# Performance work log

Measured on AMD Instinct MI355X. Metric: run time of the kernel, lower is better.

The kernel has to match this reference:

```python
import jax, jax.numpy as jnp
import numpy as np

H, D = 8, 32  # gat_num_heads, structure_feature_dim // heads
N_CFG, E_CFG = 20000, 320000
N_DFG, E_DFG = 20000, 320000


def _gat(x, src, dst, lin, a_s, a_d, b):
    # PyG GATConv (concat=True), inference (dropout off). src/dst include self-loops.
    N = x.shape[0]
    xw = (x @ lin).reshape(N, H, D)              # [N,H,D]
    sc_s = (xw * a_s).sum(-1)                    # [N,H] att_src scores
    sc_d = (xw * a_d).sum(-1)                    # [N,H] att_dst scores
    alpha = jax.nn.leaky_relu(sc_s[src] + sc_d[dst], 0.2)   # [E,H]
    m = jax.lax.stop_gradient(jax.ops.segment_max(alpha, dst, num_segments=N))
    e = jnp.exp(alpha - m[dst])
    s = jax.ops.segment_sum(e, dst, num_segments=N)
    w = e / s[dst]                               # softmax over incoming edges per dst
    out = jax.ops.segment_sum(xw[src] * w[..., None], dst, num_segments=N)
    return out.reshape(N, H * D) + b


def _gat_stack(x, ei, params):
    N = x.shape[0]
    loops = jnp.arange(N)
    src = jnp.concatenate([ei[0], loops])        # add_self_loops=True (PyG default)
    dst = jnp.concatenate([ei[1], loops])
    for p in params:
        x = jax.nn.relu(_gat(x, src, dst, *p))
    return x.mean(0, keepdims=True)              # global_mean_pool -> [1, 256]


def _mha(x, in_w, in_b, out_w, out_b):
    # torch nn.MultiheadAttention, seq_len=1, batch=1, x:[1,256]
    qkv = x @ in_w.T + in_b                      # [1, 3*256]
    q, k, v = jnp.split(qkv, 3, axis=-1)
    q = q.reshape(1, H, D); k = k.reshape(1, H, D); v = v.reshape(1, H, D)
    scores = (q * k).sum(-1, keepdims=True) / jnp.sqrt(jnp.float32(D))
    attn = jax.nn.softmax(scores, axis=0)        # key length 1
    return (attn * v).reshape(1, H * D) @ out_w.T + out_b


def setup_inputs():
    key = jax.random.key(0)
    ks = iter(jax.random.split(key, 40))
    d = {}
    d['cfg_x'] = jax.random.normal(next(ks), (N_CFG, 64), jnp.float32)
    d['dfg_x'] = jax.random.normal(next(ks), (N_DFG, 32), jnp.float32)
    d['cfg_ei'] = jax.random.randint(next(ks), (2, E_CFG), 0, N_CFG)
    d['dfg_ei'] = jax.random.randint(next(ks), (2, E_DFG), 0, N_DFG)
    for name, in0 in (('cfg', 64), ('dfg', 32)):
        for i in range(3):
            fi = in0 if i == 0 else H * D
            s = 1.0 / np.sqrt(fi)
            d[f'{name}_lin{i}'] = jax.random.normal(next(ks), (fi, H * D), jnp.float32) * s
            d[f'{name}_as{i}'] = jax.random.normal(next(ks), (H, D), jnp.float32) * s
            d[f'{name}_ad{i}'] = jax.random.normal(next(ks), (H, D), jnp.float32) * s
            d[f'{name}_b{i}'] = jnp.zeros((H * D,), jnp.float32)
    E = H * D
    d['mha_in_w'] = jax.random.normal(next(ks), (3 * E, E), jnp.float32) / np.sqrt(E)
    d['mha_in_b'] = jnp.zeros((3 * E,), jnp.float32)
    d['mha_out_w'] = jax.random.normal(next(ks), (E, E), jnp.float32) / np.sqrt(E)
    d['mha_out_b'] = jnp.zeros((E,), jnp.float32)
    d['fus_w'] = jax.random.normal(next(ks), (E, 2 * E), jnp.float32) / np.sqrt(2 * E)
    d['fus_b'] = jnp.zeros((E,), jnp.float32)
    return d


def reference(cfg_x, dfg_x, cfg_ei, dfg_ei,
              cfg_lin0, cfg_as0, cfg_ad0, cfg_b0,
              cfg_lin1, cfg_as1, cfg_ad1, cfg_b1,
              cfg_lin2, cfg_as2, cfg_ad2, cfg_b2,
              dfg_lin0, dfg_as0, dfg_ad0, dfg_b0,
              dfg_lin1, dfg_as1, dfg_ad1, dfg_b1,
              dfg_lin2, dfg_as2, dfg_ad2, dfg_b2,
              mha_in_w, mha_in_b, mha_out_w, mha_out_b, fus_w, fus_b):
    cfg_p = [(cfg_lin0, cfg_as0, cfg_ad0, cfg_b0),
             (cfg_lin1, cfg_as1, cfg_ad1, cfg_b1),
             (cfg_lin2, cfg_as2, cfg_ad2, cfg_b2)]
    dfg_p = [(dfg_lin0, dfg_as0, dfg_ad0, dfg_b0),
             (dfg_lin1, dfg_as1, dfg_ad1, dfg_b1),
             (dfg_lin2, dfg_as2, dfg_ad2, dfg_b2)]
    cfg_f = _mha(_gat_stack(cfg_x, cfg_ei, cfg_p), mha_in_w, mha_in_b, mha_out_w, mha_out_b)
    dfg_f = _mha(_gat_stack(dfg_x, dfg_ei, dfg_p), mha_in_w, mha_in_b, mha_out_w, mha_out_b)
    return jnp.concatenate([cfg_f, dfg_f], axis=1) @ fus_w.T + fus_b
```

## Files before the change

kernel.cpp:

```cpp
#include <hip/hip_runtime.h>

#define NN 20000
#define ER 320000
#define ET 340000
#define CC 256
#define HH 8
#define DD 32


__global__ void zero_k(int* cnt, float* pooled) {
  int t = blockIdx.x * 256 + threadIdx.x;
  if (t < NN) cnt[t] = 0;
  if (pooled && t < 2 * CC) pooled[t] = 0.f;
}


__global__ void hist_k(const int* __restrict__ ei, int* __restrict__ cnt) {
  int e = blockIdx.x * 256 + threadIdx.x;
  if (e >= ET) return;
  int dst = (e < ER) ? ei[ER + e] : (e - ER);
  atomicAdd(&cnt[dst], 1);
}

__global__ __launch_bounds__(1024) void scan_k(const int* __restrict__ cnt,
                                               int* __restrict__ offs,
                                               int* __restrict__ cur) {
  __shared__ int part[1024];
  int t = threadIdx.x;
  const int CH = (NN + 1023) / 1024;
  int b = t * CH; if (b > NN) b = NN;
  int e = b + CH; if (e > NN) e = NN;
  int s = 0;
  for (int i = b; i < e; ++i) s += cnt[i];
  part[t] = s;
  __syncthreads();
  for (int off = 1; off < 1024; off <<= 1) {
    int v = (t >= off) ? part[t - off] : 0;
    __syncthreads();
    part[t] += v;
    __syncthreads();
  }
  int run = (t > 0) ? part[t - 1] : 0;
  for (int i = b; i < e; ++i) {
    int c = cnt[i];
    offs[i] = run;
    cur[i] = run;
    run += c;
  }
  if (t == 0) offs[NN] = ET;
}

__global__ void scatter_k(const int* __restrict__ ei, int* __restrict__ cur,
                          int* __restrict__ csr_src, int* __restrict__ csr_dst) {
  int e = blockIdx.x * 256 + threadIdx.x;
  if (e >= ET) return;
  int src, dst;
  if (e < ER) { src = ei[e]; dst = ei[ER + e]; }
  else        { src = dst = e - ER; }
  int pos = atomicAdd(&cur[dst], 1);
  csr_src[pos] = src;
  csr_dst[pos] = dst;
}

__global__ __launch_bounds__(256) void gemm_k(const float* __restrict__ X,
                                              const float* __restrict__ W,
                                              float* __restrict__ O, int K) {
  __shared__ float As[2][16][68];
  __shared__ float Bs[2][16][68];
  int tid = threadIdx.x;
  int tx = tid & 15;
  int ty = tid >> 4;
  int rb = blockIdx.y * 64, cb = blockIdx.x * 64;

  int arow = tid & 63;
  int akc = (tid >> 6) * 4;
  int bkk = tid >> 4;
  int bcol = (tid & 15) * 4;
  int gr = rb + arow; if (gr >= NN) gr = NN - 1;

  float acc[4][4] = {};
  float4 ar, br;
  int nk = K >> 4;

#define GLOAD(k0)                                                     \
  do {                                                                \
    ar = *(const float4*)&X[(size_t)gr * K + (k0) + akc];             \
    br = *(const float4*)&W[(size_t)((k0) + bkk) * CC + cb + bcol];   \
  } while (0)

#define LWRITE(buf)                                                   \
  do {                                                                \
    As[buf][akc][arow] = ar.x; As[buf][akc + 1][arow] = ar.y;         \
    As[buf][akc + 2][arow] = ar.z; As[buf][akc + 3][arow] = ar.w;     \
    *(float4*)&Bs[buf][bkk][bcol] = br;                               \
  } while (0)

  GLOAD(0);
  LWRITE(0);
  __syncthreads();
  int cur = 0;
  for (int t = 0; t < nk; ++t) {
    if (t + 1 < nk) GLOAD((t + 1) << 4);
#pragma unroll
    for (int kk = 0; kk < 16; ++kk) {
      float4 a = *(const float4*)&As[cur][kk][ty * 4];
      float4 b = *(const float4*)&Bs[cur][kk][tx * 4];
      acc[0][0] += a.x * b.x; acc[0][1] += a.x * b.y; acc[0][2] += a.x * b.z; acc[0][3] += a.x * b.w;
      acc[1][0] += a.y * b.x; acc[1][1] += a.y * b.y; acc[1][2] += a.y * b.z; acc[1][3] += a.y * b.w;
      acc[2][0] += a.z * b.x; acc[2][1] += a.z * b.y; acc[2][2] += a.z * b.z; acc[2][3] += a.z * b.w;
      acc[3][0] += a.w * b.x; acc[3][1] += a.w * b.y; acc[3][2] += a.w * b.z; acc[3][3] += a.w * b.w;
    }
    if (t + 1 < nk) LWRITE(cur ^ 1);
    __syncthreads();
    cur ^= 1;
  }
#undef GLOAD
#undef LWRITE

#pragma unroll
  for (int i = 0; i < 4; ++i) {
    int r = rb + ty * 4 + i;
    if (r < NN) {
      *(float4*)&O[(size_t)r * CC + cb + tx * 4] =
          make_float4(acc[i][0], acc[i][1], acc[i][2], acc[i][3]);
    }
  }
}

__global__ void scores_k(const float* __restrict__ xw, const float* __restrict__ a_s,
                         const float* __restrict__ a_d, float* __restrict__ scs,
                         float* __restrict__ scd) {
  int t = blockIdx.x * blockDim.x + threadIdx.x;
  if (t >= NN * HH) return;
  int h = t & 7, n = t >> 3;
  const float* row = xw + (size_t)n * CC + h * DD;
  const float* as = a_s + h * DD;
  const float* ad = a_d + h * DD;
  float ss = 0.f, sd = 0.f;
#pragma unroll
  for (int d = 0; d < DD; ++d) {
    float v = row[d];
    ss += v * as[d];
    sd += v * ad[d];
  }
  scs[t] = ss;
  scd[t] = sd;
}

__global__ void alpha_k(const int* __restrict__ csr_src, const int* __restrict__ csr_dst,
                        const float* __restrict__ scs, const float* __restrict__ scd,
                        float* __restrict__ alpha) {
  int p = blockIdx.x * 256 + threadIdx.x;
  if (p >= ET) return;
  int s = csr_src[p], d = csr_dst[p];
  const float4* s4 = (const float4*)(scs + (size_t)s * 8);
  const float4* d4 = (const float4*)(scd + (size_t)d * 8);
  float4 a0 = s4[0], a1 = s4[1];
  float4 b0 = d4[0], b1 = d4[1];
  float4 r0, r1;
  float v;
  v = a0.x + b0.x; r0.x = v > 0.f ? v : 0.2f * v;
  v = a0.y + b0.y; r0.y = v > 0.f ? v : 0.2f * v;
  v = a0.z + b0.z; r0.z = v > 0.f ? v : 0.2f * v;
  v = a0.w + b0.w; r0.w = v > 0.f ? v : 0.2f * v;
  v = a1.x + b1.x; r1.x = v > 0.f ? v : 0.2f * v;
  v = a1.y + b1.y; r1.y = v > 0.f ? v : 0.2f * v;
  v = a1.z + b1.z; r1.z = v > 0.f ? v : 0.2f * v;
  v = a1.w + b1.w; r1.w = v > 0.f ? v : 0.2f * v;
  float4* o4 = (float4*)(alpha + (size_t)p * 8);
  o4[0] = r0; o4[1] = r1;
}

__global__ __launch_bounds__(256) void stats_k(const float* __restrict__ alpha,
                                               const int* __restrict__ offs,
                                               float* __restrict__ ms,
                                               float* __restrict__ inv) {
  int wid = (blockIdx.x * 256 + threadIdx.x) >> 6;
  if (wid >= NN) return;
  int lane = threadIdx.x & 63;
  int j = lane >> 3, h = lane & 7;
  int beg = offs[wid], end = offs[wid + 1];
  float m = -1e30f;
  for (int p = beg + j; p < end; p += 8)
    m = fmaxf(m, alpha[(size_t)p * 8 + h]);
#pragma unroll
  for (int off = 8; off <= 32; off <<= 1)
    m = fmaxf(m, __shfl_xor(m, off, 64));
  float s = 0.f;
  for (int p = beg + j; p < end; p += 8)
    s += __expf(alpha[(size_t)p * 8 + h] - m);
#pragma unroll
  for (int off = 8; off <= 32; off <<= 1)
    s += __shfl_xor(s, off, 64);
  if (lane < 8) {
    ms[(size_t)wid * 8 + h] = m;
    inv[(size_t)wid * 8 + h] = 1.f / s;
  }
}

__global__ __launch_bounds__(256) void aggr_k(const float* __restrict__ xw,
                                              const float* __restrict__ alpha,
                                              const float* __restrict__ ms,
                                              const float* __restrict__ inv,
                                              const int* __restrict__ csr,
                                              const int* __restrict__ offs,
                                              const float* __restrict__ bias,
                                              float* __restrict__ out) {
  int n = blockIdx.x;
  int tid = threadIdx.x;
  int h = tid >> 5;
  int beg = offs[n], end = offs[n + 1];
  float m = ms[(size_t)n * 8 + h];
  float iv = inv[(size_t)n * 8 + h];
  float acc = 0.f;
  int p = beg;
  for (; p + 8 <= end; p += 8) {
    int s[8]; float wv[8]; float x[8];
#pragma unroll
    for (int i = 0; i < 8; ++i) s[i] = csr[p + i];
#pragma unroll
    for (int i = 0; i < 8; ++i) wv[i] = alpha[(size_t)(p + i) * 8 + h];
#pragma unroll
    for (int i = 0; i < 8; ++i) x[i] = xw[(size_t)s[i] * CC + tid];
#pragma unroll
    for (int i = 0; i < 8; ++i) acc += __expf(wv[i] - m) * iv * x[i];
  }
  for (; p + 4 <= end; p += 4) {
    int s[4]; float wv[4]; float x[4];
#pragma unroll
    for (int i = 0; i < 4; ++i) s[i] = csr[p + i];
#pragma unroll
    for (int i = 0; i < 4; ++i) wv[i] = alpha[(size_t)(p + i) * 8 + h];
#pragma unroll
    for (int i = 0; i < 4; ++i) x[i] = xw[(size_t)s[i] * CC + tid];
#pragma unroll
    for (int i = 0; i < 4; ++i) acc += __expf(wv[i] - m) * iv * x[i];
  }
  for (; p < end; ++p)
    acc += __expf(alpha[(size_t)p * 8 + h] - m) * iv * xw[(size_t)csr[p] * CC + tid];
  float r = acc + bias[tid];
  out[(size_t)n * CC + tid] = (r > 0.f) ? r : 0.f;
}

__global__ void pool_k(const float* __restrict__ x, float* __restrict__ pooled) {
  int tid = threadIdx.x;
  int rb = blockIdx.x * 50;
  float acc = 0.f;
  for (int r = 0; r < 50; ++r) acc += x[(size_t)(rb + r) * CC + tid];
  atomicAdd(&pooled[tid], acc * (1.f / NN));
}

__global__ __launch_bounds__(256) void head12_k(const float* __restrict__ x,
                                                const float* __restrict__ W,
                                                const float* __restrict__ b,
                                                float* __restrict__ y) {
  int o = (blockIdx.x * 256 + threadIdx.x) >> 6;
  if (o >= 512) return;
  int lane = threadIdx.x & 63;
  int g = o >> 8, t = o & 255;
  float4 wv = *(const float4*)&W[(size_t)t * 256 + lane * 4];
  float4 xv = *(const float4*)&x[g * 256 + lane * 4];
  float s = wv.x * xv.x + wv.y * xv.y + wv.z * xv.z + wv.w * xv.w;
#pragma unroll
  for (int off = 32; off >= 1; off >>= 1) s += __shfl_xor(s, off, 64);
  if (lane == 0) y[o] = s + b[t];
}

__global__ __launch_bounds__(256) void head3_k(const float* __restrict__ f,
                                               const float* __restrict__ W,
                                               const float* __restrict__ b,
                                               float* __restrict__ out) {
  int o = (blockIdx.x * 256 + threadIdx.x) >> 6;
  if (o >= 256) return;
  int lane = threadIdx.x & 63;
  const float* wr = W + (size_t)o * 512;
  float4 w0 = *(const float4*)&wr[lane * 4];
  float4 w1 = *(const float4*)&wr[lane * 4 + 256];
  float4 f0 = *(const float4*)&f[lane * 4];
  float4 f1 = *(const float4*)&f[lane * 4 + 256];
  float s = w0.x * f0.x + w0.y * f0.y + w0.z * f0.z + w0.w * f0.w +
            w1.x * f1.x + w1.y * f1.y + w1.z * f1.z + w1.w * f1.w;
#pragma unroll
  for (int off = 32; off >= 1; off >>= 1) s += __shfl_xor(s, off, 64);
  if (lane == 0) out[o] = s + b[o];
}

extern "C" void kernel_launch(void* const* d_in, const int* in_sizes, int n_in,
                              void* d_out, int out_size, void* d_ws, size_t ws_size,
                              hipStream_t stream) {
  const float* cfg_x = (const float*)d_in[0];
  const float* dfg_x = (const float*)d_in[1];
  const int* cfg_ei = (const int*)d_in[2];
  const int* dfg_ei = (const int*)d_in[3];
  const float *lin[2][3], *as_[2][3], *ad_[2][3], *bs_[2][3];
  for (int g = 0; g < 2; ++g)
    for (int i = 0; i < 3; ++i) {
      int base = 4 + g * 12 + i * 4;
      lin[g][i] = (const float*)d_in[base];
      as_[g][i] = (const float*)d_in[base + 1];
      ad_[g][i] = (const float*)d_in[base + 2];
      bs_[g][i] = (const float*)d_in[base + 3];
    }
  const float* mha_in_w = (const float*)d_in[28];
  const float* mha_in_b = (const float*)d_in[29];
  const float* mha_out_w = (const float*)d_in[30];
  const float* mha_out_b = (const float*)d_in[31];
  const float* fus_w = (const float*)d_in[32];
  const float* fus_b = (const float*)d_in[33];
  float* outp = (float*)d_out;

  char* w = (char*)d_ws;
  size_t o = 0;
  auto alloc = [&](size_t bytes) -> char* {
    char* p = w + o;
    o += (bytes + 255) & ~(size_t)255;
    return p;
  };
  float* bufA = (float*)alloc((size_t)NN * CC * 4);
  float* bufB = (float*)alloc((size_t)NN * CC * 4);
  float* scs = (float*)alloc((size_t)NN * HH * 4);
  float* scd = (float*)alloc((size_t)NN * HH * 4);
  float* ms = (float*)alloc((size_t)NN * HH * 4);
  float* inv = (float*)alloc((size_t)NN * HH * 4);
  float* alpha = (float*)alloc((size_t)ET * HH * 4);
  int* csr = (int*)alloc((size_t)ET * 4);
  int* csrd = (int*)alloc((size_t)ET * 4);
  int* offs = (int*)alloc((size_t)(NN + 1) * 4);
  int* cnt = (int*)alloc((size_t)NN * 4);
  int* cur = (int*)alloc((size_t)NN * 4);
  float* pooled = (float*)alloc(2 * CC * 4);
  float* vbuf = (float*)alloc(2 * CC * 4);
  float* fbuf = (float*)alloc(2 * CC * 4);

  const int* ei[2] = {cfg_ei, dfg_ei};
  const float* xin[2] = {cfg_x, dfg_x};
  const int K0[2] = {64, 32};

  for (int g = 0; g < 2; ++g) {
    zero_k<<<(NN + 255) / 256, 256, 0, stream>>>(cnt, g == 0 ? pooled : nullptr);
    hist_k<<<(ET + 255) / 256, 256, 0, stream>>>(ei[g], cnt);
    scan_k<<<1, 1024, 0, stream>>>(cnt, offs, cur);
    scatter_k<<<(ET + 255) / 256, 256, 0, stream>>>(ei[g], cur, csr, csrd);

    const float* x = xin[g];
    for (int l = 0; l < 3; ++l) {
      int K = (l == 0) ? K0[g] : CC;
      dim3 grid(CC / 64, (NN + 63) / 64);
      gemm_k<<<grid, 256, 0, stream>>>(x, lin[g][l], bufA, K);
      scores_k<<<(NN * HH + 255) / 256, 256, 0, stream>>>(bufA, as_[g][l], ad_[g][l],
                                                          scs, scd);
      alpha_k<<<(ET + 255) / 256, 256, 0, stream>>>(csr, csrd, scs, scd, alpha);
      stats_k<<<(NN * 64 + 255) / 256, 256, 0, stream>>>(alpha, offs, ms, inv);
      aggr_k<<<NN, 256, 0, stream>>>(bufA, alpha, ms, inv, csr, offs, bs_[g][l], bufB);
      x = bufB;
    }
    pool_k<<<(NN / 50), 256, 0, stream>>>(bufB, pooled + g * CC);
  }
  head12_k<<<128, 256, 0, stream>>>(pooled, mha_in_w + 512 * 256, mha_in_b + 512, vbuf);
  head12_k<<<128, 256, 0, stream>>>(vbuf, mha_out_w, mha_out_b, fbuf);
  head3_k<<<64, 256, 0, stream>>>(fbuf, fus_w, fus_b, outp);
}
```

Baseline: 930.9 us.

## Fuse attention scores into GEMM epilogue and alpha computation into softmax stats

Computes the per-head source and destination attention scores in the GEMM epilogue with warp shuffles, which removes the separate scores kernel and its re-read of the projected features. The leaky-relu alpha computation moves into the per-destination stats kernel, gathering source scores through the CSR, so the alpha kernel and the csr_dst array are no longer needed. This drops two launches per layer and some memory traffic. In exchange, the stats kernel now does scattered gathers, and the GEMM epilogue relies on each head's 32 columns mapping onto 8 adjacent lanes.

```diff
diff --git a/kernel.cpp b/kernel.cpp
--- a/kernel.cpp
+++ b/kernel.cpp
@@ -51,7 +51,7 @@
 }
 
 __global__ void scatter_k(const int* __restrict__ ei, int* __restrict__ cur,
-                          int* __restrict__ csr_src, int* __restrict__ csr_dst) {
+                          int* __restrict__ csr_src) {
   int e = blockIdx.x * 256 + threadIdx.x;
   if (e >= ET) return;
   int src, dst;
@@ -59,12 +59,15 @@
   else        { src = dst = e - ER; }
   int pos = atomicAdd(&cur[dst], 1);
   csr_src[pos] = src;
-  csr_dst[pos] = dst;
 }
 
 __global__ __launch_bounds__(256) void gemm_k(const float* __restrict__ X,
                                               const float* __restrict__ W,
-                                              float* __restrict__ O, int K) {
+                                              float* __restrict__ O, int K,
+                                              const float* __restrict__ a_s,
+                                              const float* __restrict__ a_d,
+                                              float* __restrict__ scs,
+                                              float* __restrict__ scd) {
   __shared__ float As[2][16][68];
   __shared__ float Bs[2][16][68];
   int tid = threadIdx.x;
@@ -125,54 +128,39 @@
           make_float4(acc[i][0], acc[i][1], acc[i][2], acc[i][3]);
     }
   }
-}
-
-__global__ void scores_k(const float* __restrict__ xw, const float* __restrict__ a_s,
-                         const float* __restrict__ a_d, float* __restrict__ scs,
-                         float* __restrict__ scd) {
-  int t = blockIdx.x * blockDim.x + threadIdx.x;
-  if (t >= NN * HH) return;
-  int h = t & 7, n = t >> 3;
-  const float* row = xw + (size_t)n * CC + h * DD;
-  const float* as = a_s + h * DD;
-  const float* ad = a_d + h * DD;
-  float ss = 0.f, sd = 0.f;
-#pragma unroll
-  for (int d = 0; d < DD; ++d) {
-    float v = row[d];
-    ss += v * as[d];
-    sd += v * ad[d];
-  }
-  scs[t] = ss;
-  scd[t] = sd;
-}
-
-__global__ void alpha_k(const int* __restrict__ csr_src, const int* __restrict__ csr_dst,
-                        const float* __restrict__ scs, const float* __restrict__ scd,
-                        float* __restrict__ alpha) {
-  int p = blockIdx.x * 256 + threadIdx.x;
-  if (p >= ET) return;
-  int s = csr_src[p], d = csr_dst[p];
-  const float4* s4 = (const float4*)(scs + (size_t)s * 8);
-  const float4* d4 = (const float4*)(scd + (size_t)d * 8);
-  float4 a0 = s4[0], a1 = s4[1];
-  float4 b0 = d4[0], b1 = d4[1];
-  float4 r0, r1;
-  float v;
-  v = a0.x + b0.x; r0.x = v > 0.f ? v : 0.2f * v;
-  v = a0.y + b0.y; r0.y = v > 0.f ? v : 0.2f * v;
-  v = a0.z + b0.z; r0.z = v > 0.f ? v : 0.2f * v;
-  v = a0.w + b0.w; r0.w = v > 0.f ? v : 0.2f * v;
-  v = a1.x + b1.x; r1.x = v > 0.f ? v : 0.2f * v;
-  v = a1.y + b1.y; r1.y = v > 0.f ? v : 0.2f * v;
-  v = a1.z + b1.z; r1.z = v > 0.f ? v : 0.2f * v;
-  v = a1.w + b1.w; r1.w = v > 0.f ? v : 0.2f * v;
-  float4* o4 = (float4*)(alpha + (size_t)p * 8);
-  o4[0] = r0; o4[1] = r1;
-}
-
-__global__ __launch_bounds__(256) void stats_k(const float* __restrict__ alpha,
+
+  {
+    int h = 2 * blockIdx.x + (tx >> 3);
+    int dbase = (tx & 7) * 4;
+    const float* asp = a_s + h * DD + dbase;
+    const float* adp = a_d + h * DD + dbase;
+    float as0 = asp[0], as1 = asp[1], as2 = asp[2], as3 = asp[3];
+    float ad0 = adp[0], ad1 = adp[1], ad2 = adp[2], ad3 = adp[3];
+#pragma unroll
+    for (int i = 0; i < 4; ++i) {
+      float ps = acc[i][0] * as0 + acc[i][1] * as1 + acc[i][2] * as2 + acc[i][3] * as3;
+      float pd = acc[i][0] * ad0 + acc[i][1] * ad1 + acc[i][2] * ad2 + acc[i][3] * ad3;
+#pragma unroll
+      for (int off = 1; off <= 4; off <<= 1) {
+        ps += __shfl_xor(ps, off, 64);
+        pd += __shfl_xor(pd, off, 64);
+      }
+      if ((tx & 7) == 0) {
+        int r = rb + ty * 4 + i;
+        if (r < NN) {
+          scs[(size_t)r * 8 + h] = ps;
+          scd[(size_t)r * 8 + h] = pd;
+        }
+      }
+    }
+  }
+}
+
+__global__ __launch_bounds__(256) void stats_k(const float* __restrict__ scs,
+                                               const float* __restrict__ scd,
+                                               const int* __restrict__ csr,
                                                const int* __restrict__ offs,
+                                               float* __restrict__ alpha,
                                                float* __restrict__ ms,
                                                float* __restrict__ inv) {
   int wid = (blockIdx.x * 256 + threadIdx.x) >> 6;
@@ -180,21 +168,27 @@
   int lane = threadIdx.x & 63;
   int j = lane >> 3, h = lane & 7;
   int beg = offs[wid], end = offs[wid + 1];
+  float sd = scd[(size_t)wid * 8 + h];
   float m = -1e30f;
-  for (int p = beg + j; p < end; p += 8)
-    m = fmaxf(m, alpha[(size_t)p * 8 + h]);
+  for (int p = beg + j; p < end; p += 8) {
+    int s = csr[p];
+    float a = scs[(size_t)s * 8 + h] + sd;
+    a = (a > 0.f) ? a : 0.2f * a;
+    alpha[(size_t)p * 8 + h] = a;
+    m = fmaxf(m, a);
+  }
 #pragma unroll
   for (int off = 8; off <= 32; off <<= 1)
     m = fmaxf(m, __shfl_xor(m, off, 64));
-  float s = 0.f;
+  float ssum = 0.f;
   for (int p = beg + j; p < end; p += 8)
-    s += __expf(alpha[(size_t)p * 8 + h] - m);
+    ssum += __expf(alpha[(size_t)p * 8 + h] - m);
 #pragma unroll
   for (int off = 8; off <= 32; off <<= 1)
-    s += __shfl_xor(s, off, 64);
+    ssum += __shfl_xor(ssum, off, 64);
   if (lane < 8) {
     ms[(size_t)wid * 8 + h] = m;
-    inv[(size_t)wid * 8 + h] = 1.f / s;
+    inv[(size_t)wid * 8 + h] = 1.f / ssum;
   }
 }
 
@@ -324,7 +318,6 @@
   float* inv = (float*)alloc((size_t)NN * HH * 4);
   float* alpha = (float*)alloc((size_t)ET * HH * 4);
   int* csr = (int*)alloc((size_t)ET * 4);
-  int* csrd = (int*)alloc((size_t)ET * 4);
   int* offs = (int*)alloc((size_t)(NN + 1) * 4);
   int* cnt = (int*)alloc((size_t)NN * 4);
   int* cur = (int*)alloc((size_t)NN * 4);
@@ -340,17 +333,16 @@
     zero_k<<<(NN + 255) / 256, 256, 0, stream>>>(cnt, g == 0 ? pooled : nullptr);
     hist_k<<<(ET + 255) / 256, 256, 0, stream>>>(ei[g], cnt);
     scan_k<<<1, 1024, 0, stream>>>(cnt, offs, cur);
-    scatter_k<<<(ET + 255) / 256, 256, 0, stream>>>(ei[g], cur, csr, csrd);
+    scatter_k<<<(ET + 255) / 256, 256, 0, stream>>>(ei[g], cur, csr);
 
     const float* x = xin[g];
     for (int l = 0; l < 3; ++l) {
       int K = (l == 0) ? K0[g] : CC;
       dim3 grid(CC / 64, (NN + 63) / 64);
-      gemm_k<<<grid, 256, 0, stream>>>(x, lin[g][l], bufA, K);
-      scores_k<<<(NN * HH + 255) / 256, 256, 0, stream>>>(bufA, as_[g][l], ad_[g][l],
-                                                          scs, scd);
-      alpha_k<<<(ET + 255) / 256, 256, 0, stream>>>(csr, csrd, scs, scd, alpha);
-      stats_k<<<(NN * 64 + 255) / 256, 256, 0, stream>>>(alpha, offs, ms, inv);
+      gemm_k<<<grid, 256, 0, stream>>>(x, lin[g][l], bufA, K,
+                                       as_[g][l], ad_[g][l], scs, scd);
+      stats_k<<<(NN * 64 + 255) / 256, 256, 0, stream>>>(scs, scd, csr, offs,
+                                                         alpha, ms, inv);
       aggr_k<<<NN, 256, 0, stream>>>(bufA, alpha, ms, inv, csr, offs, bs_[g][l], bufB);
       x = bufB;
     }
```

New measurement: 869.7 us. 6.6% less time.
